# Performance work log

Measured on AMD Instinct MI355X. Metric: run time of the kernel, lower is better.

Reference implementation:

```python
import jax, jax.numpy as jnp
import numpy as np

N_NODES = 50000
NEG_SLOPE = 0.2  # PyG GATConv default
EPS = 1e-16      # PyG softmax denominator epsilon


def gat_conv(x, W, att_src, att_dst, bias, src, dst, heads, out_ch):
    # x: [N, F_in]; W: [F_in, heads*out_ch]; att_*: [heads, out_ch]
    N = x.shape[0]
    h = (x @ W).reshape(N, heads, out_ch)              # [N,H,C]
    a_src = jnp.sum(h * att_src, axis=-1)              # [N,H]
    a_dst = jnp.sum(h * att_dst, axis=-1)              # [N,H]
    alpha = a_src[src] + a_dst[dst]                    # [E,H]
    alpha = jnp.where(alpha > 0, alpha, NEG_SLOPE * alpha)  # leaky_relu
    amax = jax.ops.segment_max(alpha, dst, num_segments=N)  # [N,H]
    amax = jnp.where(jnp.isfinite(amax), amax, 0.0)
    ex = jnp.exp(alpha - amax[dst])                    # [E,H]
    denom = jax.ops.segment_sum(ex, dst, num_segments=N)    # [N,H]
    coef = ex / (denom[dst] + EPS)                     # [E,H]
    msg = h[src] * coef[:, :, None]                    # [E,H,C]
    out = jax.ops.segment_sum(msg, dst, num_segments=N)     # [N,H,C]
    return out.reshape(N, heads * out_ch) + bias


def setup_inputs() -> dict:
    key = jax.random.key(0)
    ks = jax.random.split(key, 11)
    T, N, F = 8, N_NODES, 64
    E = 1_600_000
    x = jax.random.normal(ks[0], (T, N, F), dtype=jnp.float32)
    edge_index = jax.random.randint(ks[1], (2, E), 0, N, dtype=jnp.int64)
    s = 0.1
    return {
        "x": x,
        "edge_index": edge_index,
        "W1": jax.random.normal(ks[2], (F, 64), jnp.float32) * s,
        "att_src1": jax.random.normal(ks[3], (8, 8), jnp.float32) * s,
        "att_dst1": jax.random.normal(ks[4], (8, 8), jnp.float32) * s,
        "bias1": jax.random.normal(ks[5], (64,), jnp.float32) * s,
        "W2": jax.random.normal(ks[6], (64, F), jnp.float32) * s,
        "att_src2": jax.random.normal(ks[7], (1, F), jnp.float32) * s,
        "att_dst2": jax.random.normal(ks[8], (1, F), jnp.float32) * s,
        "bias2": jax.random.normal(ks[9], (F,), jnp.float32) * s,
    }


def reference(x, edge_index, W1, att_src1, att_dst1, bias1, W2, att_src2, att_dst2, bias2):
    N = x.shape[1]
    # PyG GATConv adds self-loops by default
    loops = jnp.arange(N, dtype=edge_index.dtype)
    src = jnp.concatenate([edge_index[0], loops])
    dst = jnp.concatenate([edge_index[1], loops])

    def step(xt):  # xt: [N, F] ; dropout is identity in eval mode
        y = jax.nn.elu(gat_conv(xt, W1, att_src1, att_dst1, bias1, src, dst, 8, 8))
        y = gat_conv(y, W2, att_src2, att_dst2, bias2, src, dst, 1, xt.shape[-1])
        return jax.nn.log_softmax(y, axis=-1)

    return jax.vmap(step)(x)  # [T, N, F]
```

## Files before the change

### kernel.cpp

```cpp
#include <hip/hip_runtime.h>
#include <hip/hip_bf16.h>
#include <math.h>


typedef __hip_bfloat16 bf16;

#define TILES  16
#define TSHIFT 12

__device__ __forceinline__ float bf2f(unsigned short u) {
    return __uint_as_float(((unsigned int)u) << 16);
}


__global__ __launch_bounds__(256) void count2_kernel(const int* __restrict__ srcs,
                                                     const int* __restrict__ dsts,
                                                     int* cnt2, int E) {
    int i = blockIdx.x * 256 + threadIdx.x;
    if (i < E) atomicAdd(&cnt2[dsts[i] * TILES + (srcs[i] >> TSHIFT)], 1);
}

__device__ __forceinline__ int bucket_val(const int* __restrict__ cnt2, int idx, int M) {
    if (idx >= M) return 0;
    int n = idx >> 4, tile = idx & (TILES - 1);
    return cnt2[idx] + ((tile == (n >> TSHIFT)) ? 1 : 0);
}

__global__ __launch_bounds__(256) void scanA_kernel(const int* __restrict__ cnt2,
                                                    int* bsum, int M) {
    __shared__ int sd[256];
    int tid = threadIdx.x;
    int idx = blockIdx.x * 256 + tid;
    int v = bucket_val(cnt2, idx, M);
    sd[tid] = v;
    __syncthreads();
    for (int off = 128; off > 0; off >>= 1) {
        if (tid < off) sd[tid] += sd[tid + off];
        __syncthreads();
    }
    if (tid == 0) bsum[blockIdx.x] = sd[0];
}

__global__ __launch_bounds__(1024) void scanB_kernel(const int* __restrict__ bsum,
                                                     int* boff, int B) {
    __shared__ int ls[1024];
    int t = threadIdx.x;
    int chunk = (B + 1023) / 1024;
    int b = t * chunk;
    int sum = 0;
    for (int i = 0; i < chunk; ++i) {
        int idx = b + i;
        if (idx < B) sum += bsum[idx];
    }
    ls[t] = sum;
    __syncthreads();
    for (int off = 1; off < 1024; off <<= 1) {
        int v = (t >= off) ? ls[t - off] : 0;
        __syncthreads();
        ls[t] += v;
        __syncthreads();
    }
    int run = (t == 0) ? 0 : ls[t - 1];
    for (int i = 0; i < chunk; ++i) {
        int idx = b + i;
        if (idx < B) {
            boff[idx] = run;
            run += bsum[idx];
        }
    }
}

__global__ __launch_bounds__(256) void scanC_kernel(const int* __restrict__ cnt2,
                                                    const int* __restrict__ boff,
                                                    int* cur2, int* rowp, int M, int N) {
    __shared__ int sd[256];
    int tid = threadIdx.x;
    int idx = blockIdx.x * 256 + tid;
    int v = bucket_val(cnt2, idx, M);
    sd[tid] = v;
    __syncthreads();
    for (int off = 1; off < 256; off <<= 1) {
        int t = (tid >= off) ? sd[tid - off] : 0;
        __syncthreads();
        sd[tid] += t;
        __syncthreads();
    }
    int inc = sd[tid];
    int go  = boff[blockIdx.x] + inc - v;
    if (idx < M) {
        cur2[idx] = go;
        if ((idx & (TILES - 1)) == 0) rowp[idx >> 4] = go;
        if (idx == M - 1) rowp[N] = go + v;
    }
}

__global__ __launch_bounds__(256) void fill2_kernel(const int* __restrict__ srcs,
                                                    const int* __restrict__ dsts,
                                                    int* cur2, int* esrc, int E, int N) {
    int i = blockIdx.x * 256 + threadIdx.x;
    if (i >= E + N) return;
    int s, d;
    if (i < E) { s = srcs[i]; d = dsts[i]; }
    else       { s = i - E;   d = s; }
    int pos = atomicAdd(&cur2[d * TILES + (s >> TSHIFT)], 1);
    esrc[pos] = s;
}


__device__ __forceinline__ float4 ld4(const float* p) { return *(const float4*)p; }
__device__ __forceinline__ float4 ld4(const bf16* p) {
    ushort4 u = *(const ushort4*)p;
    float4 r;
    r.x = bf2f(u.x); r.y = bf2f(u.y); r.z = bf2f(u.z); r.w = bf2f(u.w);
    return r;
}


template <typename TIN, int H, int C>
__global__ __launch_bounds__(256) void gemm_att_kernel(
    const TIN* __restrict__ xin,
    size_t node_stride, size_t t_stride,
    const float* __restrict__ Wm,
    const float* __restrict__ att_s,
    const float* __restrict__ att_d,
    bf16* __restrict__ hout,
    float* __restrict__ asrc,
    float* __restrict__ adst,
    int N) {
    __shared__ float Ws[64 * 64];
    int tid = threadIdx.x;
    {
        const float4* W4 = (const float4*)Wm;
        float4* Ws4 = (float4*)Ws;
#pragma unroll
        for (int i = 0; i < 4; ++i) Ws4[tid + 256 * i] = W4[tid + 256 * i];
    }
    __syncthreads();

    int c  = tid & 63;
    int wv = tid >> 6;
    int t0 = blockIdx.y * 4;
    int n  = blockIdx.x * 4 + wv;
    if (n >= N) return;

    const TIN* xb = xin + (size_t)n * node_stride + (size_t)t0 * t_stride;
    float acc[4] = {0.f, 0.f, 0.f, 0.f};

#pragma unroll 2
    for (int k4 = 0; k4 < 16; ++k4) {
        float4 xv[4];
#pragma unroll
        for (int r = 0; r < 4; ++r)
            xv[r] = ld4(xb + (size_t)r * t_stride + k4 * 4);
        float w0 = Ws[(4 * k4 + 0) * 64 + c];
        float w1 = Ws[(4 * k4 + 1) * 64 + c];
        float w2 = Ws[(4 * k4 + 2) * 64 + c];
        float w3 = Ws[(4 * k4 + 3) * 64 + c];
#pragma unroll
        for (int r = 0; r < 4; ++r) {
            acc[r] = fmaf(xv[r].x, w0, acc[r]);
            acc[r] = fmaf(xv[r].y, w1, acc[r]);
            acc[r] = fmaf(xv[r].z, w2, acc[r]);
            acc[r] = fmaf(xv[r].w, w3, acc[r]);
        }
    }

    float as_w = att_s[c];
    float ad_w = att_d[c];
    bf16*  hn  = hout + (size_t)n * 512;
    float* asn = asrc + (size_t)n * (8 * H);
    float* adn = adst + (size_t)n * (8 * H);
#pragma unroll
    for (int r = 0; r < 4; ++r) {
        int tt = t0 + r;
        float a = acc[r];
        hn[tt * 64 + c] = __float2bfloat16(a);
        float vs = a * as_w;
        float vd = a * ad_w;
#pragma unroll
        for (int off = 1; off < C; off <<= 1) {
            vs += __shfl_xor(vs, off, 64);
            vd += __shfl_xor(vd, off, 64);
        }
        if ((c % C) == 0) {
            int hd = c / C;
            asn[tt * H + hd] = vs;
            adn[tt * H + hd] = vd;
        }
    }
}


#define SWZ(PU, Q) __uint_as_float(__builtin_amdgcn_ds_swizzle((PU), ((Q) << 5) | 0x18))

template <int H, bool FINAL>
__global__ __launch_bounds__(256) void gat_edge_kernel(
    const bf16* __restrict__ h_all,
    const float* __restrict__ asrc_all,
    const float* __restrict__ adst_all,
    const int* __restrict__ row,
    const int* __restrict__ esrc,
    const float* __restrict__ bias,
    bf16* __restrict__ outb,
    float* __restrict__ outf,
    int N) {
    int tid  = threadIdx.x;
    int lane = tid & 63;
    int t0   = blockIdx.y * 4;
    int n    = blockIdx.x * 4 + (tid >> 6);
    if (n >= N) return;

    const char* asrcb = (const char*)asrc_all;
    const unsigned short* hb = (const unsigned short*)h_all;

    const int head = (H == 8) ? (lane >> 3) : 0;
    float adn[4];
#pragma unroll
    for (int i = 0; i < 4; ++i)
        adn[i] = adst_all[(size_t)n * (8 * H) + (t0 + i) * H + head];

    int e0  = row[n];
    int deg = row[n + 1] - e0;
    int toff = t0 * 64 + lane;

    float lsum[4] = {0.f, 0.f, 0.f, 0.f};
    float acc[4]  = {0.f, 0.f, 0.f, 0.f};

    for (int base = 0; base < deg; base += 64) {
        int cnt = deg - base; if (cnt > 64) cnt = 64;
        int sv = (lane < cnt) ? esrc[e0 + base + lane] : 0;

        if constexpr (H == 8) {
            unsigned head4 = (unsigned)(head << 2);
            unsigned l7_4  = (unsigned)((lane & 7) << 2);
#pragma unroll
            for (int sub = 0; sub < 8; ++sub) {
                if (sub * 8 >= cnt) break;
                int svj = __builtin_amdgcn_ds_bpermute(sub * 32 + l7_4, sv);
                unsigned abase = (((unsigned)svj) << 8) | head4;
                bool valid = (sub * 8 + (lane & 7) < cnt);
                float p[4];
#pragma unroll
                for (int i = 0; i < 4; ++i) {
                    float av = *(const float*)(asrcb + (abase | ((unsigned)(t0 + i) << 5)));
                    float tv = av + adn[i];
                    tv = tv > 0.f ? tv : 0.2f * tv;
                    tv = valid ? tv : -INFINITY;
                    p[i] = __expf(tv);
                    lsum[i] += p[i];
                }
                unsigned pu0 = __float_as_uint(p[0]);
                unsigned pu1 = __float_as_uint(p[1]);
                unsigned pu2 = __float_as_uint(p[2]);
                unsigned pu3 = __float_as_uint(p[3]);
#define ACC_EDGE(Q)                                                            \
    {                                                                          \
        unsigned sj = (unsigned)__builtin_amdgcn_readlane(sv, sub * 8 + (Q));  \
        const unsigned short* hrow = hb + ((size_t)sj << 9) + toff;            \
        acc[0] = fmaf(SWZ(pu0, Q), bf2f(hrow[0]),   acc[0]);                   \
        acc[1] = fmaf(SWZ(pu1, Q), bf2f(hrow[64]),  acc[1]);                   \
        acc[2] = fmaf(SWZ(pu2, Q), bf2f(hrow[128]), acc[2]);                   \
        acc[3] = fmaf(SWZ(pu3, Q), bf2f(hrow[192]), acc[3]);                   \
    }
                ACC_EDGE(0) ACC_EDGE(1) ACC_EDGE(2) ACC_EDGE(3)
                ACC_EDGE(4) ACC_EDGE(5) ACC_EDGE(6) ACC_EDGE(7)
#undef ACC_EDGE
            }
        } else {
            unsigned abase = ((unsigned)sv) << 5;
            float p[4];
#pragma unroll
            for (int i = 0; i < 4; ++i) {
                float av = *(const float*)(asrcb + (abase | ((unsigned)(t0 + i) << 2)));
                float tv = av + adn[i];
                tv = tv > 0.f ? tv : 0.2f * tv;
                tv = (lane < cnt) ? tv : -INFINITY;
                p[i] = __expf(tv);
                lsum[i] += p[i];
            }
            for (int j0 = 0; j0 < cnt; j0 += 8) {
#pragma unroll
                for (int q = 0; q < 8; ++q) {
                    int j = j0 + q;
                    unsigned sj = (unsigned)__builtin_amdgcn_readlane(sv, j);
                    const unsigned short* hrow = hb + ((size_t)sj << 9) + toff;
                    float pj0 = __uint_as_float(
                        __builtin_amdgcn_readlane(__float_as_uint(p[0]), j));
                    float pj1 = __uint_as_float(
                        __builtin_amdgcn_readlane(__float_as_uint(p[1]), j));
                    float pj2 = __uint_as_float(
                        __builtin_amdgcn_readlane(__float_as_uint(p[2]), j));
                    float pj3 = __uint_as_float(
                        __builtin_amdgcn_readlane(__float_as_uint(p[3]), j));
                    acc[0] = fmaf(pj0, bf2f(hrow[0]),   acc[0]);
                    acc[1] = fmaf(pj1, bf2f(hrow[64]),  acc[1]);
                    acc[2] = fmaf(pj2, bf2f(hrow[128]), acc[2]);
                    acc[3] = fmaf(pj3, bf2f(hrow[192]), acc[3]);
                }
            }
        }
    }

#pragma unroll
    for (int i = 0; i < 4; ++i) {
        float ls = lsum[i];
        if constexpr (H == 8) {
            ls += __shfl_xor(ls, 1, 64);
            ls += __shfl_xor(ls, 2, 64);
            ls += __shfl_xor(ls, 4, 64);
        } else {
#pragma unroll
            for (int o = 1; o < 64; o <<= 1) ls += __shfl_xor(ls, o, 64);
        }
        float v = acc[i] / (ls + 1e-16f) + bias[lane];
        if (!FINAL) {
            float y = v > 0.f ? v : expm1f(v);
            outb[(size_t)n * 512 + (t0 + i) * 64 + lane] = __float2bfloat16(y);
        } else {
            float mx = v;
#pragma unroll
            for (int off = 1; off < 64; off <<= 1) mx = fmaxf(mx, __shfl_xor(mx, off, 64));
            float ex = __expf(v - mx);
            float sm = ex;
#pragma unroll
            for (int off = 1; off < 64; off <<= 1) sm += __shfl_xor(sm, off, 64);
            outf[(size_t)(t0 + i) * N * 64 + (size_t)n * 64 + lane] =
                (v - mx) - __logf(sm);
        }
    }
}


extern "C" void kernel_launch(void* const* d_in, const int* in_sizes, int n_in,
                              void* d_out, int out_size, void* d_ws, size_t ws_size,
                              hipStream_t stream) {
    const float* x        = (const float*)d_in[0];
    const int*   eidx     = (const int*)d_in[1];
    const float* W1       = (const float*)d_in[2];
    const float* att_src1 = (const float*)d_in[3];
    const float* att_dst1 = (const float*)d_in[4];
    const float* bias1    = (const float*)d_in[5];
    const float* W2       = (const float*)d_in[6];
    const float* att_src2 = (const float*)d_in[7];
    const float* att_dst2 = (const float*)d_in[8];
    const float* bias2    = (const float*)d_in[9];
    float* dout = (float*)d_out;

    const int N = 50000;
    const int F = 64;
    const int E = in_sizes[1] / 2;
    const int T = in_sizes[0] / (N * F);
    const int NT = T * N;
    const int Etot = E + N;
    const int BPT = (N + 3) / 4;
    const int M  = N * TILES;
    const int SB = (M + 255) / 256;

    const int* srcs = eidx;
    const int* dsts = eidx + E;

    char* ws = (char*)d_ws;
    size_t off = 0;
    auto carve = [&](size_t bytes) -> void* {
        void* p = ws + off;
        off = (off + bytes + 255) & ~(size_t)255;
        return p;
    };
    bf16*  h_all  = (bf16*)carve((size_t)NT * 64 * sizeof(bf16));
    bf16*  y1_all = (bf16*)carve((size_t)NT * 64 * sizeof(bf16));
    float* asrc   = (float*)carve((size_t)NT * 8 * sizeof(float));
    float* adst   = (float*)carve((size_t)NT * 8 * sizeof(float));
    int*   rowp   = (int*)carve((size_t)(N + 1) * sizeof(int));
    int*   cnt2   = (int*)carve((size_t)M * sizeof(int));
    int*   cur2   = (int*)carve((size_t)M * sizeof(int));
    int*   bsum   = (int*)carve((size_t)SB * sizeof(int));
    int*   boff   = (int*)carve((size_t)SB * sizeof(int));
    int*   esrc   = (int*)carve((size_t)Etot * sizeof(int));
    (void)ws_size;

    hipMemsetAsync(cnt2, 0, (size_t)M * sizeof(int), stream);
    count2_kernel<<<(E + 255) / 256, 256, 0, stream>>>(srcs, dsts, cnt2, E);
    scanA_kernel<<<SB, 256, 0, stream>>>(cnt2, bsum, M);
    scanB_kernel<<<1, 1024, 0, stream>>>(bsum, boff, SB);
    scanC_kernel<<<SB, 256, 0, stream>>>(cnt2, boff, cur2, rowp, M, N);
    fill2_kernel<<<(E + N + 255) / 256, 256, 0, stream>>>(srcs, dsts, cur2, esrc, E, N);

    dim3 ggrid((N + 3) / 4, 2);
    dim3 egrid(BPT, T / 4);
    gemm_att_kernel<float, 8, 8><<<ggrid, 256, 0, stream>>>(
        x, 64, (size_t)N * 64, W1, att_src1, att_dst1, h_all, asrc, adst, N);
    gat_edge_kernel<8, false><<<egrid, 256, 0, stream>>>(
        h_all, asrc, adst, rowp, esrc, bias1, y1_all, nullptr, N);
    gemm_att_kernel<bf16, 1, 64><<<ggrid, 256, 0, stream>>>(
        y1_all, 512, 64, W2, att_src2, att_dst2, h_all, asrc, adst, N);
    gat_edge_kernel<1, true><<<egrid, 256, 0, stream>>>(
        h_all, asrc, adst, rowp, esrc, bias2, nullptr, dout, N);
}
```

Measured before the change: 1.068 ms.

## Process all eight timesteps per wave and store attention-source scores in bf16

The edge kernel now handles all 8 timesteps in one wave instead of splitting them across two grid rows of 4. The edge list, index reads and row offsets are loaded once per node, and each gathered h row is read as a full 1 KB contiguous block. The source attention scores are stored in bf16 and laid out head-major with time innermost, so one 16-byte load fetches all 8 timesteps per source node. The cost is a halved grid, double the accumulator registers (risking occupancy), and reduced precision in the attention logits.

```diff
diff --git a/kernel.cpp b/kernel.cpp
--- a/kernel.cpp
+++ b/kernel.cpp
@@ -10,6 +10,16 @@
 
 __device__ __forceinline__ float bf2f(unsigned short u) {
     return __uint_as_float(((unsigned int)u) << 16);
+}
+__device__ __forceinline__ float lo16(int u) {
+    return __uint_as_float(((unsigned)u) << 16);
+}
+__device__ __forceinline__ float hi16(int u) {
+    return __uint_as_float(((unsigned)u) & 0xFFFF0000u);
+}
+__device__ __forceinline__ unsigned short f2bfu(float f) {
+    bf16 b = __float2bfloat16(f);
+    return *reinterpret_cast<unsigned short*>(&b);
 }
 
 
@@ -124,7 +134,7 @@
     const float* __restrict__ att_s,
     const float* __restrict__ att_d,
     bf16* __restrict__ hout,
-    float* __restrict__ asrc,
+    unsigned short* __restrict__ asrc,
     float* __restrict__ adst,
     int N) {
     __shared__ float Ws[64 * 64];
@@ -168,8 +178,8 @@
     float as_w = att_s[c];
     float ad_w = att_d[c];
     bf16*  hn  = hout + (size_t)n * 512;
-    float* asn = asrc + (size_t)n * (8 * H);
-    float* adn = adst + (size_t)n * (8 * H);
+    unsigned short* asn = asrc + (size_t)n * (H * 8);
+    float* adn = adst + (size_t)n * (H * 8);
 #pragma unroll
     for (int r = 0; r < 4; ++r) {
         int tt = t0 + r;
@@ -184,19 +194,19 @@
         }
         if ((c % C) == 0) {
             int hd = c / C;
-            asn[tt * H + hd] = vs;
-            adn[tt * H + hd] = vd;
-        }
-    }
-}
-
-
-#define SWZ(PU, Q) __uint_as_float(__builtin_amdgcn_ds_swizzle((PU), ((Q) << 5) | 0x18))
+            asn[hd * 8 + tt] = f2bfu(vs);
+            adn[hd * 8 + tt] = vd;
+        }
+    }
+}
+
+
+#define SWZ(PF, Q) __uint_as_float(__builtin_amdgcn_ds_swizzle(__float_as_uint(PF), ((Q) << 5) | 0x18))
 
 template <int H, bool FINAL>
 __global__ __launch_bounds__(256) void gat_edge_kernel(
     const bf16* __restrict__ h_all,
-    const float* __restrict__ asrc_all,
+    const unsigned short* __restrict__ asrc_all,
     const float* __restrict__ adst_all,
     const int* __restrict__ row,
     const int* __restrict__ esrc,
@@ -206,104 +216,110 @@
     int N) {
     int tid  = threadIdx.x;
     int lane = tid & 63;
-    int t0   = blockIdx.y * 4;
     int n    = blockIdx.x * 4 + (tid >> 6);
     if (n >= N) return;
 
     const char* asrcb = (const char*)asrc_all;
     const unsigned short* hb = (const unsigned short*)h_all;
-
     const int head = (H == 8) ? (lane >> 3) : 0;
-    float adn[4];
-#pragma unroll
-    for (int i = 0; i < 4; ++i)
-        adn[i] = adst_all[(size_t)n * (8 * H) + (t0 + i) * H + head];
+
+    float adn[8];
+    {
+        const float* adp = adst_all + (size_t)n * (H * 8) + head * 8;
+        float4 d0 = ld4(adp), d1 = ld4(adp + 4);
+        adn[0] = d0.x; adn[1] = d0.y; adn[2] = d0.z; adn[3] = d0.w;
+        adn[4] = d1.x; adn[5] = d1.y; adn[6] = d1.z; adn[7] = d1.w;
+    }
 
     int e0  = row[n];
     int deg = row[n + 1] - e0;
-    int toff = t0 * 64 + lane;
-
-    float lsum[4] = {0.f, 0.f, 0.f, 0.f};
-    float acc[4]  = {0.f, 0.f, 0.f, 0.f};
+
+    float lsum[8] = {0.f, 0.f, 0.f, 0.f, 0.f, 0.f, 0.f, 0.f};
+    float acc[8]  = {0.f, 0.f, 0.f, 0.f, 0.f, 0.f, 0.f, 0.f};
 
     for (int base = 0; base < deg; base += 64) {
         int cnt = deg - base; if (cnt > 64) cnt = 64;
         int sv = (lane < cnt) ? esrc[e0 + base + lane] : 0;
 
         if constexpr (H == 8) {
-            unsigned head4 = (unsigned)(head << 2);
-            unsigned l7_4  = (unsigned)((lane & 7) << 2);
+            unsigned head16 = (unsigned)(head << 4);
+            unsigned l7_4   = (unsigned)((lane & 7) << 2);
 #pragma unroll
             for (int sub = 0; sub < 8; ++sub) {
                 if (sub * 8 >= cnt) break;
                 int svj = __builtin_amdgcn_ds_bpermute(sub * 32 + l7_4, sv);
-                unsigned abase = (((unsigned)svj) << 8) | head4;
+                int4 a16 = *(const int4*)(asrcb + ((((unsigned)svj) << 7) | head16));
                 bool valid = (sub * 8 + (lane & 7) < cnt);
-                float p[4];
-#pragma unroll
-                for (int i = 0; i < 4; ++i) {
-                    float av = *(const float*)(asrcb + (abase | ((unsigned)(t0 + i) << 5)));
-                    float tv = av + adn[i];
-                    tv = tv > 0.f ? tv : 0.2f * tv;
-                    tv = valid ? tv : -INFINITY;
-                    p[i] = __expf(tv);
-                    lsum[i] += p[i];
+                float p[8];
+                {
+                    float at[8] = {lo16(a16.x), hi16(a16.x), lo16(a16.y), hi16(a16.y),
+                                   lo16(a16.z), hi16(a16.z), lo16(a16.w), hi16(a16.w)};
+#pragma unroll
+                    for (int t = 0; t < 8; ++t) {
+                        float tv = at[t] + adn[t];
+                        tv = tv > 0.f ? tv : 0.2f * tv;
+                        tv = valid ? tv : -INFINITY;
+                        p[t] = __expf(tv);
+                        lsum[t] += p[t];
+                    }
                 }
-                unsigned pu0 = __float_as_uint(p[0]);
-                unsigned pu1 = __float_as_uint(p[1]);
-                unsigned pu2 = __float_as_uint(p[2]);
-                unsigned pu3 = __float_as_uint(p[3]);
 #define ACC_EDGE(Q)                                                            \
     {                                                                          \
         unsigned sj = (unsigned)__builtin_amdgcn_readlane(sv, sub * 8 + (Q));  \
-        const unsigned short* hrow = hb + ((size_t)sj << 9) + toff;            \
-        acc[0] = fmaf(SWZ(pu0, Q), bf2f(hrow[0]),   acc[0]);                   \
-        acc[1] = fmaf(SWZ(pu1, Q), bf2f(hrow[64]),  acc[1]);                   \
-        acc[2] = fmaf(SWZ(pu2, Q), bf2f(hrow[128]), acc[2]);                   \
-        acc[3] = fmaf(SWZ(pu3, Q), bf2f(hrow[192]), acc[3]);                   \
+        const unsigned short* hrow = hb + ((size_t)sj << 9) + lane;            \
+        acc[0] = fmaf(SWZ(p[0], Q), bf2f(hrow[0]),   acc[0]);                  \
+        acc[1] = fmaf(SWZ(p[1], Q), bf2f(hrow[64]),  acc[1]);                  \
+        acc[2] = fmaf(SWZ(p[2], Q), bf2f(hrow[128]), acc[2]);                  \
+        acc[3] = fmaf(SWZ(p[3], Q), bf2f(hrow[192]), acc[3]);                  \
+        acc[4] = fmaf(SWZ(p[4], Q), bf2f(hrow[256]), acc[4]);                  \
+        acc[5] = fmaf(SWZ(p[5], Q), bf2f(hrow[320]), acc[5]);                  \
+        acc[6] = fmaf(SWZ(p[6], Q), bf2f(hrow[384]), acc[6]);                  \
+        acc[7] = fmaf(SWZ(p[7], Q), bf2f(hrow[448]), acc[7]);                  \
     }
                 ACC_EDGE(0) ACC_EDGE(1) ACC_EDGE(2) ACC_EDGE(3)
                 ACC_EDGE(4) ACC_EDGE(5) ACC_EDGE(6) ACC_EDGE(7)
 #undef ACC_EDGE
             }
         } else {
-            unsigned abase = ((unsigned)sv) << 5;
-            float p[4];
-#pragma unroll
-            for (int i = 0; i < 4; ++i) {
-                float av = *(const float*)(asrcb + (abase | ((unsigned)(t0 + i) << 2)));
-                float tv = av + adn[i];
-                tv = tv > 0.f ? tv : 0.2f * tv;
-                tv = (lane < cnt) ? tv : -INFINITY;
-                p[i] = __expf(tv);
-                lsum[i] += p[i];
+            int4 a16 = *(const int4*)(asrcb + (((unsigned)sv) << 4));
+            float p[8];
+            {
+                float at[8] = {lo16(a16.x), hi16(a16.x), lo16(a16.y), hi16(a16.y),
+                               lo16(a16.z), hi16(a16.z), lo16(a16.w), hi16(a16.w)};
+#pragma unroll
+                for (int t = 0; t < 8; ++t) {
+                    float tv = at[t] + adn[t];
+                    tv = tv > 0.f ? tv : 0.2f * tv;
+                    tv = (lane < cnt) ? tv : -INFINITY;
+                    p[t] = __expf(tv);
+                    lsum[t] += p[t];
+                }
             }
             for (int j0 = 0; j0 < cnt; j0 += 8) {
 #pragma unroll
                 for (int q = 0; q < 8; ++q) {
                     int j = j0 + q;
                     unsigned sj = (unsigned)__builtin_amdgcn_readlane(sv, j);
-                    const unsigned short* hrow = hb + ((size_t)sj << 9) + toff;
-                    float pj0 = __uint_as_float(
-                        __builtin_amdgcn_readlane(__float_as_uint(p[0]), j));
-                    float pj1 = __uint_as_float(
-                        __builtin_amdgcn_readlane(__float_as_uint(p[1]), j));
-                    float pj2 = __uint_as_float(
-                        __builtin_amdgcn_readlane(__float_as_uint(p[2]), j));
-                    float pj3 = __uint_as_float(
-                        __builtin_amdgcn_readlane(__float_as_uint(p[3]), j));
-                    acc[0] = fmaf(pj0, bf2f(hrow[0]),   acc[0]);
-                    acc[1] = fmaf(pj1, bf2f(hrow[64]),  acc[1]);
-                    acc[2] = fmaf(pj2, bf2f(hrow[128]), acc[2]);
-                    acc[3] = fmaf(pj3, bf2f(hrow[192]), acc[3]);
+                    const unsigned short* hrow = hb + ((size_t)sj << 9) + lane;
+#define PJ(T) __uint_as_float(__builtin_amdgcn_readlane(__float_as_uint(p[T]), j))
+                    acc[0] = fmaf(PJ(0), bf2f(hrow[0]),   acc[0]);
+                    acc[1] = fmaf(PJ(1), bf2f(hrow[64]),  acc[1]);
+                    acc[2] = fmaf(PJ(2), bf2f(hrow[128]), acc[2]);
+                    acc[3] = fmaf(PJ(3), bf2f(hrow[192]), acc[3]);
+                    acc[4] = fmaf(PJ(4), bf2f(hrow[256]), acc[4]);
+                    acc[5] = fmaf(PJ(5), bf2f(hrow[320]), acc[5]);
+                    acc[6] = fmaf(PJ(6), bf2f(hrow[384]), acc[6]);
+                    acc[7] = fmaf(PJ(7), bf2f(hrow[448]), acc[7]);
+#undef PJ
                 }
             }
         }
     }
 
-#pragma unroll
-    for (int i = 0; i < 4; ++i) {
-        float ls = lsum[i];
+    float bi = bias[lane];
+#pragma unroll
+    for (int t = 0; t < 8; ++t) {
+        float ls = lsum[t];
         if constexpr (H == 8) {
             ls += __shfl_xor(ls, 1, 64);
             ls += __shfl_xor(ls, 2, 64);
@@ -312,10 +328,10 @@
 #pragma unroll
             for (int o = 1; o < 64; o <<= 1) ls += __shfl_xor(ls, o, 64);
         }
-        float v = acc[i] / (ls + 1e-16f) + bias[lane];
+        float v = acc[t] / (ls + 1e-16f) + bi;
         if (!FINAL) {
             float y = v > 0.f ? v : expm1f(v);
-            outb[(size_t)n * 512 + (t0 + i) * 64 + lane] = __float2bfloat16(y);
+            outb[(size_t)n * 512 + t * 64 + lane] = __float2bfloat16(y);
         } else {
             float mx = v;
 #pragma unroll
@@ -324,7 +340,7 @@
             float sm = ex;
 #pragma unroll
             for (int off = 1; off < 64; off <<= 1) sm += __shfl_xor(sm, off, 64);
-            outf[(size_t)(t0 + i) * N * 64 + (size_t)n * 64 + lane] =
+            outf[(size_t)t * N * 64 + (size_t)n * 64 + lane] =
                 (v - mx) - __logf(sm);
         }
     }
@@ -368,7 +384,7 @@
     };
     bf16*  h_all  = (bf16*)carve((size_t)NT * 64 * sizeof(bf16));
     bf16*  y1_all = (bf16*)carve((size_t)NT * 64 * sizeof(bf16));
-    float* asrc   = (float*)carve((size_t)NT * 8 * sizeof(float));
+    unsigned short* asrc = (unsigned short*)carve((size_t)NT * 8 * sizeof(unsigned short));
     float* adst   = (float*)carve((size_t)NT * 8 * sizeof(float));
     int*   rowp   = (int*)carve((size_t)(N + 1) * sizeof(int));
     int*   cnt2   = (int*)carve((size_t)M * sizeof(int));
@@ -386,13 +402,12 @@
     fill2_kernel<<<(E + N + 255) / 256, 256, 0, stream>>>(srcs, dsts, cur2, esrc, E, N);
 
     dim3 ggrid((N + 3) / 4, 2);
-    dim3 egrid(BPT, T / 4);
     gemm_att_kernel<float, 8, 8><<<ggrid, 256, 0, stream>>>(
         x, 64, (size_t)N * 64, W1, att_src1, att_dst1, h_all, asrc, adst, N);
-    gat_edge_kernel<8, false><<<egrid, 256, 0, stream>>>(
+    gat_edge_kernel<8, false><<<BPT, 256, 0, stream>>>(
         h_all, asrc, adst, rowp, esrc, bias1, y1_all, nullptr, N);
     gemm_att_kernel<bf16, 1, 64><<<ggrid, 256, 0, stream>>>(
         y1_all, 512, 64, W2, att_src2, att_dst2, h_all, asrc, adst, N);
-    gat_edge_kernel<1, true><<<egrid, 256, 0, stream>>>(
+    gat_edge_kernel<1, true><<<BPT, 256, 0, stream>>>(
         h_all, asrc, adst, rowp, esrc, bias2, nullptr, dout, N);
 }
```

Result: slower. 1.118 ms (+4.6%).
